# Optimization experiments

Measured on AMD Instinct MI355X. Metric: run time of the kernel, lower is better.

## Reference

```python
import jax, jax.numpy as jnp
import numpy as np

# Grid config: output_shape = [2, 40, 400, 352, 16] -> sparse_shape = [41, 400, 352]
B, Dz, Hy, Wx = 2, 41, 400, 352
N_PER = 20000          # active voxels per sample
C_IN = 128
# Strided SparseConv3d(k=3, s=2, p=1) output spatial dims
Do, Ho, Wo = (Dz + 2 - 3) // 2 + 1, (Hy + 2 - 3) // 2 + 1, (Wx + 2 - 3) // 2 + 1


def setup_inputs() -> dict:
    rng = np.random.default_rng(0)
    coors_list = []
    for b in range(B):
        # unique voxel positions per sample (z limited to original 40-deep grid)
        flat = rng.choice((Dz - 1) * Hy * Wx, size=N_PER, replace=False)
        z = flat // (Hy * Wx)
        r = flat % (Hy * Wx)
        y = r // Wx
        x = r % Wx
        coors_list.append(np.stack([np.full(N_PER, b), z, y, x], axis=1))
    coors = jnp.asarray(np.concatenate(coors_list, 0), jnp.int32)  # [N,4]

    key = jax.random.key(0)
    k1, k2, k3, k4 = jax.random.split(key, 4)
    N = B * N_PER
    voxel_features = jax.random.normal(k1, (N, C_IN), jnp.float32)
    W1 = jax.random.normal(k2, (3, 3, 3, C_IN, 16), jnp.float32) * (1.0 / np.sqrt(27 * C_IN))
    W2 = jax.random.normal(k3, (3, 3, 3, 16, 16), jnp.float32) * (1.0 / np.sqrt(27 * 16))
    W3 = jax.random.normal(k4, (3, 3, 3, 16, 32), jnp.float32) * (1.0 / np.sqrt(27 * 16))
    return dict(voxel_features=voxel_features, coors=coors, W1=W1, W2=W2, W3=W3, batch_size=B)


def _offsets():
    o = jnp.stack(jnp.meshgrid(jnp.arange(3), jnp.arange(3), jnp.arange(3), indexing='ij'), -1)
    return o.reshape(27, 3)  # [27,3] kernel taps


def reference(voxel_features, coors, W1, W2, W3, batch_size):
    N = voxel_features.shape[0]
    offs = _offsets()

    # --- rulebook: dense index grid, padded by 1 so neighbor lookups never go OOB
    grid = jnp.full((batch_size, Dz + 2, Hy + 2, Wx + 2), -1, jnp.int32)
    grid = grid.at[coors[:, 0], coors[:, 1] + 1, coors[:, 2] + 1, coors[:, 3] + 1].set(
        jnp.arange(N, dtype=jnp.int32))
    # neighbor voxel index for every active site and every 3x3x3 tap: [N,27]
    nbr = grid[coors[:, 0:1], coors[:, 1:2] + offs[:, 0], coors[:, 2:3] + offs[:, 1],
               coors[:, 3:4] + offs[:, 2]]
    valid = (nbr >= 0)[..., None]
    nbr_c = jnp.clip(nbr, 0, N - 1)

    def subm(feat, W):  # submanifold conv: gather -> GEMM, output only on active sites
        Cin, Cout = W.shape[3], W.shape[4]
        g = jnp.where(valid, feat[nbr_c], 0.0)                      # [N,27,Cin]
        return jnp.einsum('nkc,kcd->nd', g, W.reshape(27, Cin, Cout))

    x = jax.nn.relu(subm(voxel_features, W1))   # SubMConv3d(128->16) + ReLU
    x = jax.nn.relu(subm(x, W2))                # SubMConv3d(16->16, same rulebook) + ReLU

    # --- SparseConv3d(16->32, k=3, stride=2, pad=1): scatter-add into downsampled grid
    contrib = jnp.einsum('nc,kcd->nkd', x, W3.reshape(27, 16, 32))  # [N,27,32]
    oz = coors[:, 1:2] + 1 - offs[:, 0]  # p_in + pad - k, must be even and in range
    oy = coors[:, 2:3] + 1 - offs[:, 1]
    ox = coors[:, 3:4] + 1 - offs[:, 2]
    pz, py, px = oz // 2, oy // 2, ox // 2
    ok = ((oz % 2 == 0) & (oy % 2 == 0) & (ox % 2 == 0) &
          (pz >= 0) & (pz < Do) & (py >= 0) & (py < Ho) & (px >= 0) & (px < Wo))
    total = batch_size * Do * Ho * Wo
    flat = coors[:, 0:1] * (Do * Ho * Wo) + pz * (Ho * Wo) + py * Wo + px
    flat = jnp.where(ok, flat, total)  # invalid -> dummy slot
    out = jnp.zeros((total + 1, 32), x.dtype).at[flat.reshape(-1)].add(
        contrib.reshape(-1, 32))[:total]
    out = jax.nn.relu(out).reshape(batch_size, Do, Ho, Wo, 32)  # dense() of sparse output
    return out
```

## Files before the change

kernel.cpp:

```cpp
#include <hip/hip_runtime.h>

#define B_   2
#define DZ   41
#define HY   400
#define WX   352
#define NVOX 40000
#define PD   43
#define PH   402
#define PW   354
#define DO_  21
#define HO_  200
#define WO_  176
#define C1   128
#define OPP  (DO_*HO_*WO_)
#define OUT_POS (B_*OPP)
#define GRID_CELLS (B_*PD*PH*PW)
#define GRID_F4  (GRID_CELLS*2/16)
#define OMASK_F4 (OUT_POS/16)


__device__ __forceinline__ int axis_taps(int pcoord, int outdim, int* ds, int* ps) {
    if (pcoord & 1) { ds[0] = 1; ps[0] = pcoord >> 1; return 1; }
    int h = pcoord >> 1, nu = 0;
    if (h < outdim) { ds[nu] = 0; ps[nu] = h; nu++; }
    ds[nu] = 2; ps[nu] = h - 1; nu++;
    return nu;
}

__global__ void k_zero(float4* __restrict__ g, float4* __restrict__ m) {
    int i = blockIdx.x * 256 + threadIdx.x;
    float4 z = make_float4(0.f, 0.f, 0.f, 0.f);
    if (i < GRID_F4)  g[i] = z;
    if (i < OMASK_F4) m[i] = z;
}

__global__ void k_build(const int* __restrict__ coors, unsigned short* __restrict__ grid,
                        unsigned char* __restrict__ omask) {
    int n = blockIdx.x * 256 + threadIdx.x;
    if (n >= NVOX) return;
    int b = coors[4*n+0], z = coors[4*n+1], y = coors[4*n+2], x = coors[4*n+3];
    int zp = z + 1, yp = y + 1, xp = x + 1;
    grid[((b*PD + zp)*PH + yp)*PW + xp] = (unsigned short)(n + 1);
    int dz[2], pz[2], dy[2], py[2], dx[2], px[2];
    int nz = axis_taps(zp, DO_, dz, pz);
    int ny = axis_taps(yp, HO_, dy, py);
    int nx = axis_taps(xp, WO_, dx, px);
    int bofs = b * OPP;
    for (int iz = 0; iz < nz; ++iz)
        for (int iy = 0; iy < ny; ++iy)
            for (int ix = 0; ix < nx; ++ix)
                omask[bofs + (pz[iz]*HO_ + py[iy])*WO_ + px[ix]] = 1;
}

__global__ void k_subm1(const float* __restrict__ feat, const float* __restrict__ W1,
                        const int* __restrict__ coors, const unsigned short* __restrict__ grid,
                        float* __restrict__ x1) {
    __shared__ int s_base[16];
    __shared__ int s_cnt[16];
    __shared__ int s_list[16][27];
    int base = blockIdx.x * 16;
    int t = threadIdx.x;
    if (t < 16) {
        int n = base + t;
        int b = coors[4*n+0], z = coors[4*n+1], y = coors[4*n+2], x = coors[4*n+3];
        s_base[t] = ((b*PD + z)*PH + y)*PW + x;
        s_cnt[t] = 0;
    }
    __syncthreads();
    for (int i = t; i < 16*27; i += 256) {
        int v = i / 27, k = i % 27;
        int dz = k / 9, dy = (k / 3) % 3, dx = k % 3;
        int id = (int)grid[s_base[v] + dz*(PH*PW) + dy*PW + dx] - 1;
        if (id >= 0) {
            int pos = atomicAdd(&s_cnt[v], 1);
            s_list[v][pos] = (k << 16) | id;
        }
    }
    __syncthreads();
    int v = t >> 4, d = t & 15;
    int cnt = s_cnt[v];
    float acc = 0.f;
    for (int tap = 0; tap < cnt; ++tap) {
        int pk = s_list[v][tap];
        int k = pk >> 16, idx = pk & 0xFFFF;
        const float4* f4 = (const float4*)(feat + (size_t)idx * C1);
        const float* w = W1 + k * (C1*16) + d;
        #pragma unroll 8
        for (int c4 = 0; c4 < 32; ++c4) {
            float4 f = f4[c4];
            acc += f.x * w[(c4*4+0)*16];
            acc += f.y * w[(c4*4+1)*16];
            acc += f.z * w[(c4*4+2)*16];
            acc += f.w * w[(c4*4+3)*16];
        }
    }
    x1[(base + v)*16 + d] = fmaxf(acc, 0.f);
}

__global__ void k_subm2(const float* __restrict__ x1, const float* __restrict__ W2,
                        const int* __restrict__ coors, const unsigned short* __restrict__ grid,
                        float* __restrict__ x2) {
    __shared__ int s_base[16];
    __shared__ int s_cnt[16];
    __shared__ int s_list[16][27];
    int base = blockIdx.x * 16;
    int t = threadIdx.x;
    if (t < 16) {
        int n = base + t;
        int b = coors[4*n+0], z = coors[4*n+1], y = coors[4*n+2], x = coors[4*n+3];
        s_base[t] = ((b*PD + z)*PH + y)*PW + x;
        s_cnt[t] = 0;
    }
    __syncthreads();
    for (int i = t; i < 16*27; i += 256) {
        int v = i / 27, k = i % 27;
        int dz = k / 9, dy = (k / 3) % 3, dx = k % 3;
        int id = (int)grid[s_base[v] + dz*(PH*PW) + dy*PW + dx] - 1;
        if (id >= 0) {
            int pos = atomicAdd(&s_cnt[v], 1);
            s_list[v][pos] = (k << 16) | id;
        }
    }
    __syncthreads();
    int v = t >> 4, d = t & 15;
    int cnt = s_cnt[v];
    float acc = 0.f;
    for (int tap = 0; tap < cnt; ++tap) {
        int pk = s_list[v][tap];
        int k = pk >> 16, idx = pk & 0xFFFF;
        const float4* xr = (const float4*)(x1 + (size_t)idx * 16);
        float4 a0 = xr[0], a1 = xr[1], a2 = xr[2], a3 = xr[3];
        const float* w = W2 + k * 256 + d;
        acc += a0.x*w[0*16]  + a0.y*w[1*16]  + a0.z*w[2*16]  + a0.w*w[3*16]
             + a1.x*w[4*16]  + a1.y*w[5*16]  + a1.z*w[6*16]  + a1.w*w[7*16]
             + a2.x*w[8*16]  + a2.y*w[9*16]  + a2.z*w[10*16] + a2.w*w[11*16]
             + a3.x*w[12*16] + a3.y*w[13*16] + a3.z*w[14*16] + a3.w*w[15*16];
    }
    x2[(base + v)*16 + d] = fmaxf(acc, 0.f);
}

__global__ void k_out(const float* __restrict__ x2, const float* __restrict__ W3,
                      const unsigned short* __restrict__ grid,
                      const unsigned char* __restrict__ omask,
                      float4* __restrict__ out4) {
    __shared__ int s_base[32];
    __shared__ int s_cnt[32];
    __shared__ int s_list[32][27];
    __shared__ unsigned char s_occ[32];
    int pbase = blockIdx.x * 32;
    int t = threadIdx.x;
    if (t < 32) {
        int p = pbase + t;
        s_occ[t] = omask[p];
        s_cnt[t] = 0;
        int b   = p / OPP,       rem = p - b * OPP;
        int pz  = rem / (HO_*WO_), r2 = rem - pz * (HO_*WO_);
        int py  = r2 / WO_,       px = r2 - py * WO_;
        s_base[t] = ((b*PD + 2*pz)*PH + 2*py)*PW + 2*px;
    }
    __syncthreads();
    for (int i = t; i < 32*27; i += 256) {
        int v = i / 27;
        if (!s_occ[v]) continue;
        int k = i % 27;
        int dz = k / 9, dy = (k / 3) % 3, dx = k % 3;
        int id = (int)grid[s_base[v] + dz*(PH*PW) + dy*PW + dx] - 1;
        if (id >= 0) {
            int pos = atomicAdd(&s_cnt[v], 1);
            s_list[v][pos] = (k << 16) | id;
        }
    }
    __syncthreads();
    int v = t >> 3, c4 = t & 7;
    float4 acc = make_float4(0.f, 0.f, 0.f, 0.f);
    if (s_occ[v]) {
        int cnt = s_cnt[v];
        for (int tap = 0; tap < cnt; ++tap) {
            int pk = s_list[v][tap];
            int k = pk >> 16, idx = pk & 0xFFFF;
            const float*  xp = x2 + (size_t)idx * 16;
            const float4* w4 = (const float4*)(W3 + k*512 + c4*4);
            #pragma unroll
            for (int c = 0; c < 16; ++c) {
                float xv = xp[c];
                float4 w = w4[c * 8];
                acc.x += xv * w.x; acc.y += xv * w.y;
                acc.z += xv * w.z; acc.w += xv * w.w;
            }
        }
        acc.x = fmaxf(acc.x, 0.f); acc.y = fmaxf(acc.y, 0.f);
        acc.z = fmaxf(acc.z, 0.f); acc.w = fmaxf(acc.w, 0.f);
    }
    out4[(size_t)(pbase + v) * 8 + c4] = acc;
}

extern "C" void kernel_launch(void* const* d_in, const int* in_sizes, int n_in,
                              void* d_out, int out_size, void* d_ws, size_t ws_size,
                              hipStream_t stream) {
    const float* feat  = (const float*)d_in[0];
    const int*   coors = (const int*)d_in[1];
    const float* W1    = (const float*)d_in[2];
    const float* W2    = (const float*)d_in[3];
    const float* W3    = (const float*)d_in[4];
    float* out = (float*)d_out;

    char* ws = (char*)d_ws;
    size_t off = 0;
    unsigned short* grid = (unsigned short*)(ws + off);
    off += (((size_t)GRID_CELLS*2) + 255) & ~(size_t)255;
    unsigned char* omask = (unsigned char*)(ws + off);
    off += ((size_t)OUT_POS + 255) & ~(size_t)255;
    float* x1 = (float*)(ws + off); off += (((size_t)NVOX*16*4) + 255) & ~(size_t)255;
    float* x2 = (float*)(ws + off);

    k_zero <<<(GRID_F4 + 255) / 256, 256, 0, stream>>>((float4*)grid, (float4*)omask);
    k_build<<<(NVOX + 255) / 256, 256, 0, stream>>>(coors, grid, omask);
    k_subm1<<<NVOX / 16, 256, 0, stream>>>(feat, W1, coors, grid, x1);
    k_subm2<<<NVOX / 16, 256, 0, stream>>>(x1, W2, coors, grid, x2);
    k_out  <<<OUT_POS / 32, 256, 0, stream>>>(x2, W3, grid, omask, (float4*)out);
}
```

Before: 341.0 us.

## Compact occupied output sites into a list and gather only those

The output conv kernel used to launch one block per 32 dense output positions and check an occupancy byte mask. Now the build kernel marks occupancy with atomicExch and appends each newly occupied output position to a compact list. A persistent grid-stride kernel then gathers only the listed positions, one warp-width of 32 channels per site. The dense output is zeroed up front in the zero kernel. This removes the pass over the roughly 1.48M mostly-empty dense positions, at the cost of global atomics in the build step, a larger int mask, and an extra float4 memset over the whole output.

```diff
diff --git a/kernel.cpp b/kernel.cpp
--- a/kernel.cpp
+++ b/kernel.cpp
@@ -15,8 +15,10 @@
 #define OPP  (DO_*HO_*WO_)
 #define OUT_POS (B_*OPP)
 #define GRID_CELLS (B_*PD*PH*PW)
+#define OUT_F4   (OUT_POS*32/4)
 #define GRID_F4  (GRID_CELLS*2/16)
-#define OMASK_F4 (OUT_POS/16)
+#define OMASK_F4 (OUT_POS/4)
+#define MAXLIST  (NVOX*8)
 
 
 __device__ __forceinline__ int axis_taps(int pcoord, int outdim, int* ds, int* ps) {
@@ -27,19 +29,22 @@
     return nu;
 }
 
-__global__ void k_zero(float4* __restrict__ g, float4* __restrict__ m) {
+__global__ void k_zero(float4* __restrict__ o, float4* __restrict__ g,
+                       float4* __restrict__ m, int* __restrict__ cntp) {
     int i = blockIdx.x * 256 + threadIdx.x;
     float4 z = make_float4(0.f, 0.f, 0.f, 0.f);
+    if (i < OUT_F4)   o[i] = z;
     if (i < GRID_F4)  g[i] = z;
     if (i < OMASK_F4) m[i] = z;
+    if (i == 0) *cntp = 0;
 }
 
 __global__ void k_build(const int* __restrict__ coors, unsigned short* __restrict__ grid,
-                        unsigned char* __restrict__ omask) {
+                        int* __restrict__ omask, int* __restrict__ list,
+                        int* __restrict__ cntp) {
     int n = blockIdx.x * 256 + threadIdx.x;
     if (n >= NVOX) return;
-    int b = coors[4*n+0], z = coors[4*n+1], y = coors[4*n+2], x = coors[4*n+3];
-    int zp = z + 1, yp = y + 1, xp = x + 1;
+    int b = coors[4*n+0], zp = coors[4*n+1] + 1, yp = coors[4*n+2] + 1, xp = coors[4*n+3] + 1;
     grid[((b*PD + zp)*PH + yp)*PW + xp] = (unsigned short)(n + 1);
     int dz[2], pz[2], dy[2], py[2], dx[2], px[2];
     int nz = axis_taps(zp, DO_, dz, pz);
@@ -48,8 +53,11 @@
     int bofs = b * OPP;
     for (int iz = 0; iz < nz; ++iz)
         for (int iy = 0; iy < ny; ++iy)
-            for (int ix = 0; ix < nx; ++ix)
-                omask[bofs + (pz[iz]*HO_ + py[iy])*WO_ + px[ix]] = 1;
+            for (int ix = 0; ix < nx; ++ix) {
+                int p = bofs + (pz[iz]*HO_ + py[iy])*WO_ + px[ix];
+                if (atomicExch(&omask[p], 1) == 0)
+                    list[atomicAdd(cntp, 1)] = p;
+            }
 }
 
 __global__ void k_subm1(const float* __restrict__ feat, const float* __restrict__ W1,
@@ -139,59 +147,59 @@
     x2[(base + v)*16 + d] = fmaxf(acc, 0.f);
 }
 
-__global__ void k_out(const float* __restrict__ x2, const float* __restrict__ W3,
-                      const unsigned short* __restrict__ grid,
-                      const unsigned char* __restrict__ omask,
-                      float4* __restrict__ out4) {
-    __shared__ int s_base[32];
-    __shared__ int s_cnt[32];
-    __shared__ int s_list[32][27];
-    __shared__ unsigned char s_occ[32];
-    int pbase = blockIdx.x * 32;
+__global__ void k_gather(const float* __restrict__ x2, const float* __restrict__ W3,
+                         const unsigned short* __restrict__ grid,
+                         const int* __restrict__ list, const int* __restrict__ cntp,
+                         float* __restrict__ out) {
+    __shared__ int s_base[8];
+    __shared__ int s_p[8];
+    __shared__ int s_cnt[8];
+    __shared__ int s_list[8][27];
+    int total = *cntp;
     int t = threadIdx.x;
-    if (t < 32) {
-        int p = pbase + t;
-        s_occ[t] = omask[p];
-        s_cnt[t] = 0;
-        int b   = p / OPP,       rem = p - b * OPP;
-        int pz  = rem / (HO_*WO_), r2 = rem - pz * (HO_*WO_);
-        int py  = r2 / WO_,       px = r2 - py * WO_;
-        s_base[t] = ((b*PD + 2*pz)*PH + 2*py)*PW + 2*px;
-    }
-    __syncthreads();
-    for (int i = t; i < 32*27; i += 256) {
-        int v = i / 27;
-        if (!s_occ[v]) continue;
-        int k = i % 27;
-        int dz = k / 9, dy = (k / 3) % 3, dx = k % 3;
-        int id = (int)grid[s_base[v] + dz*(PH*PW) + dy*PW + dx] - 1;
-        if (id >= 0) {
-            int pos = atomicAdd(&s_cnt[v], 1);
-            s_list[v][pos] = (k << 16) | id;
-        }
-    }
-    __syncthreads();
-    int v = t >> 3, c4 = t & 7;
-    float4 acc = make_float4(0.f, 0.f, 0.f, 0.f);
-    if (s_occ[v]) {
-        int cnt = s_cnt[v];
-        for (int tap = 0; tap < cnt; ++tap) {
-            int pk = s_list[v][tap];
-            int k = pk >> 16, idx = pk & 0xFFFF;
-            const float*  xp = x2 + (size_t)idx * 16;
-            const float4* w4 = (const float4*)(W3 + k*512 + c4*4);
-            #pragma unroll
-            for (int c = 0; c < 16; ++c) {
-                float xv = xp[c];
-                float4 w = w4[c * 8];
-                acc.x += xv * w.x; acc.y += xv * w.y;
-                acc.z += xv * w.z; acc.w += xv * w.w;
-            }
-        }
-        acc.x = fmaxf(acc.x, 0.f); acc.y = fmaxf(acc.y, 0.f);
-        acc.z = fmaxf(acc.z, 0.f); acc.w = fmaxf(acc.w, 0.f);
-    }
-    out4[(size_t)(pbase + v) * 8 + c4] = acc;
+    for (int e0 = blockIdx.x * 8; e0 < total; e0 += gridDim.x * 8) {
+        if (t < 8) {
+            s_cnt[t] = 0;
+            int e = e0 + t;
+            int p = (e < total) ? list[e] : -1;
+            s_p[t] = p;
+            if (p >= 0) {
+                int b  = p / OPP,        rem = p - b * OPP;
+                int pz = rem / (HO_*WO_), r2 = rem - pz * (HO_*WO_);
+                int py = r2 / WO_,        px = r2 - py * WO_;
+                s_base[t] = ((b*PD + 2*pz)*PH + 2*py)*PW + 2*px;
+            }
+        }
+        __syncthreads();
+        for (int i = t; i < 8*27; i += 256) {
+            int v = i / 27;
+            if (s_p[v] < 0) continue;
+            int k = i % 27;
+            int dz = k / 9, dy = (k / 3) % 3, dx = k % 3;
+            int id = (int)grid[s_base[v] + dz*(PH*PW) + dy*PW + dx] - 1;
+            if (id >= 0) {
+                int pos = atomicAdd(&s_cnt[v], 1);
+                s_list[v][pos] = (k << 16) | id;
+            }
+        }
+        __syncthreads();
+        int v = t >> 5, d = t & 31;
+        int p = s_p[v];
+        if (p >= 0) {
+            float acc = 0.f;
+            int cnt = s_cnt[v];
+            for (int tap = 0; tap < cnt; ++tap) {
+                int pk = s_list[v][tap];
+                int k = pk >> 16, idx = pk & 0xFFFF;
+                const float* xp = x2 + (size_t)idx * 16;
+                const float* w  = W3 + k*512 + d;
+                #pragma unroll
+                for (int c = 0; c < 16; ++c) acc += xp[c] * w[c * 32];
+            }
+            out[(size_t)p * 32 + d] = fmaxf(acc, 0.f);
+        }
+        __syncthreads();
+    }
 }
 
 extern "C" void kernel_launch(void* const* d_in, const int* in_sizes, int n_in,
@@ -208,14 +216,16 @@
     size_t off = 0;
     unsigned short* grid = (unsigned short*)(ws + off);
     off += (((size_t)GRID_CELLS*2) + 255) & ~(size_t)255;
-    unsigned char* omask = (unsigned char*)(ws + off);
-    off += ((size_t)OUT_POS + 255) & ~(size_t)255;
+    int* omask = (int*)(ws + off); off += (((size_t)OUT_POS*4) + 255) & ~(size_t)255;
+    int* list  = (int*)(ws + off); off += (((size_t)MAXLIST*4) + 255) & ~(size_t)255;
+    int* cntp  = (int*)(ws + off); off += 256;
     float* x1 = (float*)(ws + off); off += (((size_t)NVOX*16*4) + 255) & ~(size_t)255;
     float* x2 = (float*)(ws + off);
 
-    k_zero <<<(GRID_F4 + 255) / 256, 256, 0, stream>>>((float4*)grid, (float4*)omask);
-    k_build<<<(NVOX + 255) / 256, 256, 0, stream>>>(coors, grid, omask);
+    k_zero <<<(OUT_F4 + 255) / 256, 256, 0, stream>>>((float4*)out, (float4*)grid,
+                                                      (float4*)omask, cntp);
+    k_build<<<(NVOX + 255) / 256, 256, 0, stream>>>(coors, grid, omask, list, cntp);
     k_subm1<<<NVOX / 16, 256, 0, stream>>>(feat, W1, coors, grid, x1);
     k_subm2<<<NVOX / 16, 256, 0, stream>>>(x1, W2, coors, grid, x2);
-    k_out  <<<OUT_POS / 32, 256, 0, stream>>>(x2, W3, grid, omask, (float4*)out);
-}
+    k_gather<<<2048, 256, 0, stream>>>(x2, W3, grid, list, cntp, out);
+}
```

Result: slower. 394.4 us (+15.7%).

## Replace output-gather kernel with per-voxel atomic scatter plus sparse ReLU pass

Applied to the files above, without the earlier changes.

The strided output conv no longer runs one gather over every output position in the dense grid, which meant a per-position occupancy mask and neighbor lookups across the whole grid. Each active input voxel now computes its contributions to the output positions it reaches and adds them with atomicAdd. A second small kernel then applies ReLU only at the touched positions. The output buffer is zeroed with hipMemsetAsync and the occupancy mask is removed; in exchange the code adds float atomics, whose summation order is nondeterministic, and a full output memset.

```diff
diff --git a/kernel.cpp b/kernel.cpp
--- a/kernel.cpp
+++ b/kernel.cpp
@@ -13,10 +13,7 @@
 #define WO_  176
 #define C1   128
 #define OPP  (DO_*HO_*WO_)
-#define OUT_POS (B_*OPP)
 #define GRID_CELLS (B_*PD*PH*PW)
-#define GRID_F4  (GRID_CELLS*2/16)
-#define OMASK_F4 (OUT_POS/16)
 
 
 __device__ __forceinline__ int axis_taps(int pcoord, int outdim, int* ds, int* ps) {
@@ -27,29 +24,11 @@
     return nu;
 }
 
-__global__ void k_zero(float4* __restrict__ g, float4* __restrict__ m) {
-    int i = blockIdx.x * 256 + threadIdx.x;
-    float4 z = make_float4(0.f, 0.f, 0.f, 0.f);
-    if (i < GRID_F4)  g[i] = z;
-    if (i < OMASK_F4) m[i] = z;
-}
-
-__global__ void k_build(const int* __restrict__ coors, unsigned short* __restrict__ grid,
-                        unsigned char* __restrict__ omask) {
+__global__ void k_build(const int* __restrict__ coors, unsigned short* __restrict__ grid) {
     int n = blockIdx.x * 256 + threadIdx.x;
     if (n >= NVOX) return;
     int b = coors[4*n+0], z = coors[4*n+1], y = coors[4*n+2], x = coors[4*n+3];
-    int zp = z + 1, yp = y + 1, xp = x + 1;
-    grid[((b*PD + zp)*PH + yp)*PW + xp] = (unsigned short)(n + 1);
-    int dz[2], pz[2], dy[2], py[2], dx[2], px[2];
-    int nz = axis_taps(zp, DO_, dz, pz);
-    int ny = axis_taps(yp, HO_, dy, py);
-    int nx = axis_taps(xp, WO_, dx, px);
-    int bofs = b * OPP;
-    for (int iz = 0; iz < nz; ++iz)
-        for (int iy = 0; iy < ny; ++iy)
-            for (int ix = 0; ix < nx; ++ix)
-                omask[bofs + (pz[iz]*HO_ + py[iy])*WO_ + px[ix]] = 1;
+    grid[((b*PD + z+1)*PH + y+1)*PW + x+1] = (unsigned short)(n + 1);
 }
 
 __global__ void k_subm1(const float* __restrict__ feat, const float* __restrict__ W1,
@@ -139,59 +118,55 @@
     x2[(base + v)*16 + d] = fmaxf(acc, 0.f);
 }
 
-__global__ void k_out(const float* __restrict__ x2, const float* __restrict__ W3,
-                      const unsigned short* __restrict__ grid,
-                      const unsigned char* __restrict__ omask,
-                      float4* __restrict__ out4) {
-    __shared__ int s_base[32];
-    __shared__ int s_cnt[32];
-    __shared__ int s_list[32][27];
-    __shared__ unsigned char s_occ[32];
-    int pbase = blockIdx.x * 32;
-    int t = threadIdx.x;
-    if (t < 32) {
-        int p = pbase + t;
-        s_occ[t] = omask[p];
-        s_cnt[t] = 0;
-        int b   = p / OPP,       rem = p - b * OPP;
-        int pz  = rem / (HO_*WO_), r2 = rem - pz * (HO_*WO_);
-        int py  = r2 / WO_,       px = r2 - py * WO_;
-        s_base[t] = ((b*PD + 2*pz)*PH + 2*py)*PW + 2*px;
-    }
-    __syncthreads();
-    for (int i = t; i < 32*27; i += 256) {
-        int v = i / 27;
-        if (!s_occ[v]) continue;
-        int k = i % 27;
-        int dz = k / 9, dy = (k / 3) % 3, dx = k % 3;
-        int id = (int)grid[s_base[v] + dz*(PH*PW) + dy*PW + dx] - 1;
-        if (id >= 0) {
-            int pos = atomicAdd(&s_cnt[v], 1);
-            s_list[v][pos] = (k << 16) | id;
-        }
-    }
-    __syncthreads();
-    int v = t >> 3, c4 = t & 7;
-    float4 acc = make_float4(0.f, 0.f, 0.f, 0.f);
-    if (s_occ[v]) {
-        int cnt = s_cnt[v];
-        for (int tap = 0; tap < cnt; ++tap) {
-            int pk = s_list[v][tap];
-            int k = pk >> 16, idx = pk & 0xFFFF;
-            const float*  xp = x2 + (size_t)idx * 16;
-            const float4* w4 = (const float4*)(W3 + k*512 + c4*4);
-            #pragma unroll
-            for (int c = 0; c < 16; ++c) {
-                float xv = xp[c];
-                float4 w = w4[c * 8];
-                acc.x += xv * w.x; acc.y += xv * w.y;
-                acc.z += xv * w.z; acc.w += xv * w.w;
+__global__ void k_scatter(const float* __restrict__ x2, const float* __restrict__ W3,
+                          const int* __restrict__ coors, float* __restrict__ out) {
+    int v = threadIdx.x >> 5, d = threadIdx.x & 31;
+    int n = blockIdx.x * 8 + v;
+    if (n >= NVOX) return;
+    int b  = coors[4*n+0];
+    int zp = coors[4*n+1] + 1, yp = coors[4*n+2] + 1, xp = coors[4*n+3] + 1;
+    int dz[2], pz[2], dy[2], py[2], dx[2], px[2];
+    int nz = axis_taps(zp, DO_, dz, pz);
+    int ny = axis_taps(yp, HO_, dy, py);
+    int nx = axis_taps(xp, WO_, dx, px);
+    const float4* xr = (const float4*)(x2 + (size_t)n * 16);
+    float r[16];
+    *(float4*)(r + 0)  = xr[0];
+    *(float4*)(r + 4)  = xr[1];
+    *(float4*)(r + 8)  = xr[2];
+    *(float4*)(r + 12) = xr[3];
+    int bofs = b * OPP;
+    for (int iz = 0; iz < nz; ++iz)
+        for (int iy = 0; iy < ny; ++iy)
+            for (int ix = 0; ix < nx; ++ix) {
+                int k = dz[iz]*9 + dy[iy]*3 + dx[ix];
+                int p = bofs + (pz[iz]*HO_ + py[iy])*WO_ + px[ix];
+                const float* w = W3 + k*512 + d;
+                float acc = 0.f;
+                #pragma unroll
+                for (int c = 0; c < 16; ++c) acc += r[c] * w[c * 32];
+                atomicAdd(out + (size_t)p * 32 + d, acc);
             }
-        }
-        acc.x = fmaxf(acc.x, 0.f); acc.y = fmaxf(acc.y, 0.f);
-        acc.z = fmaxf(acc.z, 0.f); acc.w = fmaxf(acc.w, 0.f);
-    }
-    out4[(size_t)(pbase + v) * 8 + c4] = acc;
+}
+
+__global__ void k_relu(const int* __restrict__ coors, float* __restrict__ out) {
+    int v = threadIdx.x >> 5, d = threadIdx.x & 31;
+    int n = blockIdx.x * 8 + v;
+    if (n >= NVOX) return;
+    int b  = coors[4*n+0];
+    int zp = coors[4*n+1] + 1, yp = coors[4*n+2] + 1, xp = coors[4*n+3] + 1;
+    int dz[2], pz[2], dy[2], py[2], dx[2], px[2];
+    int nz = axis_taps(zp, DO_, dz, pz);
+    int ny = axis_taps(yp, HO_, dy, py);
+    int nx = axis_taps(xp, WO_, dx, px);
+    int bofs = b * OPP;
+    for (int iz = 0; iz < nz; ++iz)
+        for (int iy = 0; iy < ny; ++iy)
+            for (int ix = 0; ix < nx; ++ix) {
+                int p = bofs + (pz[iz]*HO_ + py[iy])*WO_ + px[ix];
+                size_t o = (size_t)p * 32 + d;
+                out[o] = fmaxf(out[o], 0.f);
+            }
 }
 
 extern "C" void kernel_launch(void* const* d_in, const int* in_sizes, int n_in,
@@ -208,14 +183,14 @@
     size_t off = 0;
     unsigned short* grid = (unsigned short*)(ws + off);
     off += (((size_t)GRID_CELLS*2) + 255) & ~(size_t)255;
-    unsigned char* omask = (unsigned char*)(ws + off);
-    off += ((size_t)OUT_POS + 255) & ~(size_t)255;
     float* x1 = (float*)(ws + off); off += (((size_t)NVOX*16*4) + 255) & ~(size_t)255;
     float* x2 = (float*)(ws + off);
 
-    k_zero <<<(GRID_F4 + 255) / 256, 256, 0, stream>>>((float4*)grid, (float4*)omask);
-    k_build<<<(NVOX + 255) / 256, 256, 0, stream>>>(coors, grid, omask);
-    k_subm1<<<NVOX / 16, 256, 0, stream>>>(feat, W1, coors, grid, x1);
-    k_subm2<<<NVOX / 16, 256, 0, stream>>>(x1, W2, coors, grid, x2);
-    k_out  <<<OUT_POS / 32, 256, 0, stream>>>(x2, W3, grid, omask, (float4*)out);
+    hipMemsetAsync(grid, 0x00, (size_t)GRID_CELLS * 2, stream);
+    hipMemsetAsync(out,  0x00, (size_t)out_size * sizeof(float), stream);
+    k_build <<<(NVOX + 255) / 256, 256, 0, stream>>>(coors, grid);
+    k_subm1 <<<NVOX / 16, 256, 0, stream>>>(feat, W1, coors, grid, x1);
+    k_subm2 <<<NVOX / 16, 256, 0, stream>>>(x1, W2, coors, grid, x2);
+    k_scatter<<<NVOX / 8, 256, 0, stream>>>(x2, W3, coors, out);
+    k_relu  <<<NVOX / 8, 256, 0, stream>>>(coors, out);
 }
```

Result: faster. 331.6 us (-2.8%).
